# Kernel optimization log

Measured on AMD Instinct MI355X. Metric: run time of the kernel, lower is better.

The kernel has to match this reference:

```python
import jax, jax.numpy as jnp
import numpy as np

N_ROWS = 5000  # hard-coded loop bound in the source
N_FEAT = 20    # hard-coded x size in the source


def setup_inputs() -> dict:
    key = jax.random.key(0)
    kA, kb, kx = jax.random.split(key, 3)
    A = jax.random.normal(kA, (N_ROWS, N_FEAT), dtype=jnp.float32)
    b = jax.random.normal(kb, (N_ROWS,), dtype=jnp.float32)
    # nn.Parameter initialized as uniform(low=1, high=13, size=20)
    x = 1.0 + 12.0 * jax.random.uniform(kx, (N_FEAT,), dtype=jnp.float32)
    return {"A": A, "b": b, "x": x}


def reference(A, b, x):
    # Original: loss = sum_i ||A[i,:] @ x - b||^2, where the scalar A[i]@x
    # broadcasts against the full vector b each iteration.
    # Vectorized: s = A @ x (shape [N_ROWS]); residual r[i,j] = s[i] - b[j].
    s = A @ x                                   # [5000]
    r = s[:, None] - b[None, :]                  # [5000, 5000] broadcasted residual
    return jnp.sum(r * r)
```

## Files before the change

### kernel.cpp

```cpp
#include <hip/hip_runtime.h>
#include <hip/hip_bf16.h>


#define N_ROWS 5000
#define N_FEAT 20
#define NBLK   20
#define BLKSZ  256
#define NWAVES (BLKSZ / 64)

__device__ __forceinline__ double wave_reduce_sum(double v) {
    #pragma unroll
    for (int off = 32; off > 0; off >>= 1)
        v += __shfl_down(v, off, 64);
    return v;
}

__global__ __launch_bounds__(BLKSZ) void lsq_partial_kernel(
        const float* __restrict__ A, const float* __restrict__ b,
        const float* __restrict__ x, double* __restrict__ ws) {
    __shared__ float xs[N_FEAT];
    if (threadIdx.x < N_FEAT) xs[threadIdx.x] = x[threadIdx.x];
    __syncthreads();

    double s1 = 0.0, s2 = 0.0, b1 = 0.0, b2 = 0.0;
    int i = blockIdx.x * BLKSZ + threadIdx.x;
    if (i < N_ROWS) {
        const float4* __restrict__ row = (const float4*)(A + (long)i * N_FEAT);
        float4 r0 = row[0], r1 = row[1], r2 = row[2], r3 = row[3], r4 = row[4];
        float bv = b[i];
        float s = r0.x * xs[0]  + r0.y * xs[1]  + r0.z * xs[2]  + r0.w * xs[3]
                + r1.x * xs[4]  + r1.y * xs[5]  + r1.z * xs[6]  + r1.w * xs[7]
                + r2.x * xs[8]  + r2.y * xs[9]  + r2.z * xs[10] + r2.w * xs[11]
                + r3.x * xs[12] + r3.y * xs[13] + r3.z * xs[14] + r3.w * xs[15]
                + r4.x * xs[16] + r4.y * xs[17] + r4.z * xs[18] + r4.w * xs[19];
        s1 = (double)s;
        s2 = (double)s * (double)s;
        b1 = (double)bv;
        b2 = (double)bv * (double)bv;
    }

    s1 = wave_reduce_sum(s1);
    s2 = wave_reduce_sum(s2);
    b1 = wave_reduce_sum(b1);
    b2 = wave_reduce_sum(b2);

    __shared__ double red[NWAVES][4];
    int lane = threadIdx.x & 63;
    int wave = threadIdx.x >> 6;
    if (lane == 0) {
        red[wave][0] = s1; red[wave][1] = s2;
        red[wave][2] = b1; red[wave][3] = b2;
    }
    __syncthreads();
    if (threadIdx.x == 0) {
        double t0 = 0, t1 = 0, t2 = 0, t3 = 0;
        #pragma unroll
        for (int w = 0; w < NWAVES; ++w) {
            t0 += red[w][0]; t1 += red[w][1];
            t2 += red[w][2]; t3 += red[w][3];
        }
        double* p = ws + 4 * blockIdx.x;
        p[0] = t0; p[1] = t1; p[2] = t2; p[3] = t3;
    }
}

__global__ __launch_bounds__(64) void lsq_finalize_kernel(
        const double* __restrict__ ws, float* __restrict__ out) {
    double s1 = 0, s2 = 0, b1 = 0, b2 = 0;
    if (threadIdx.x < NBLK) {
        const double* p = ws + 4 * threadIdx.x;
        s1 = p[0]; s2 = p[1]; b1 = p[2]; b2 = p[3];
    }
    s1 = wave_reduce_sum(s1);
    s2 = wave_reduce_sum(s2);
    b1 = wave_reduce_sum(b1);
    b2 = wave_reduce_sum(b2);
    if (threadIdx.x == 0) {
        double n = (double)N_ROWS;
        out[0] = (float)(n * s2 - 2.0 * s1 * b1 + n * b2);
    }
}

extern "C" void kernel_launch(void* const* d_in, const int* in_sizes, int n_in,
                              void* d_out, int out_size, void* d_ws, size_t ws_size,
                              hipStream_t stream) {
    const float* A = (const float*)d_in[0];
    const float* b = (const float*)d_in[1];
    const float* x = (const float*)d_in[2];
    float* out = (float*)d_out;
    double* ws = (double*)d_ws;

    lsq_partial_kernel<<<NBLK, BLKSZ, 0, stream>>>(A, b, x, ws);
    lsq_finalize_kernel<<<1, 64, 0, stream>>>(ws, out);
}
```

Before: 58.88 us.

## Fuse partial and finalize kernels using complement-checksum handshake in workspace

After: 71.18 us. 1.21x slower.

```diff
diff --git a/kernel.cpp b/kernel.cpp
--- a/kernel.cpp
+++ b/kernel.cpp
@@ -1,5 +1,4 @@
 #include <hip/hip_runtime.h>
-#include <hip/hip_bf16.h>
 
 
 #define N_ROWS 5000
@@ -8,6 +7,8 @@
 #define BLKSZ  256
 #define NWAVES (BLKSZ / 64)
 
+typedef unsigned long long u64;
+
 __device__ __forceinline__ double wave_reduce_sum(double v) {
     #pragma unroll
     for (int off = 32; off > 0; off >>= 1)
@@ -15,69 +16,99 @@
     return v;
 }
 
-__global__ __launch_bounds__(BLKSZ) void lsq_partial_kernel(
+__device__ __forceinline__ u64 d2u(double d) { return __double_as_longlong(d); }
+__device__ __forceinline__ double u2d(u64 u) { return __longlong_as_double(u); }
+
+__global__ __launch_bounds__(BLKSZ) void lsq_fused_kernel(
         const float* __restrict__ A, const float* __restrict__ b,
-        const float* __restrict__ x, double* __restrict__ ws) {
-    __shared__ float xs[N_FEAT];
-    if (threadIdx.x < N_FEAT) xs[threadIdx.x] = x[threadIdx.x];
-    __syncthreads();
+        const float* __restrict__ x, u64* __restrict__ ws,
+        float* __restrict__ out) {
+    if (blockIdx.x < NBLK) {
+        double s1 = 0.0, s2 = 0.0, b1 = 0.0, b2 = 0.0;
+        int i = blockIdx.x * BLKSZ + threadIdx.x;
+        if (i < N_ROWS) {
+            const float4* __restrict__ row = (const float4*)(A + (long)i * N_FEAT);
+            float4 r0 = row[0], r1 = row[1], r2 = row[2], r3 = row[3], r4 = row[4];
+            float bv = b[i];
+            float s = r0.x * x[0]  + r0.y * x[1]  + r0.z * x[2]  + r0.w * x[3]
+                    + r1.x * x[4]  + r1.y * x[5]  + r1.z * x[6]  + r1.w * x[7]
+                    + r2.x * x[8]  + r2.y * x[9]  + r2.z * x[10] + r2.w * x[11]
+                    + r3.x * x[12] + r3.y * x[13] + r3.z * x[14] + r3.w * x[15]
+                    + r4.x * x[16] + r4.y * x[17] + r4.z * x[18] + r4.w * x[19];
+            s1 = (double)s;
+            s2 = (double)s * (double)s;
+            b1 = (double)bv;
+            b2 = (double)bv * (double)bv;
+        }
 
-    double s1 = 0.0, s2 = 0.0, b1 = 0.0, b2 = 0.0;
-    int i = blockIdx.x * BLKSZ + threadIdx.x;
-    if (i < N_ROWS) {
-        const float4* __restrict__ row = (const float4*)(A + (long)i * N_FEAT);
-        float4 r0 = row[0], r1 = row[1], r2 = row[2], r3 = row[3], r4 = row[4];
-        float bv = b[i];
-        float s = r0.x * xs[0]  + r0.y * xs[1]  + r0.z * xs[2]  + r0.w * xs[3]
-                + r1.x * xs[4]  + r1.y * xs[5]  + r1.z * xs[6]  + r1.w * xs[7]
-                + r2.x * xs[8]  + r2.y * xs[9]  + r2.z * xs[10] + r2.w * xs[11]
-                + r3.x * xs[12] + r3.y * xs[13] + r3.z * xs[14] + r3.w * xs[15]
-                + r4.x * xs[16] + r4.y * xs[17] + r4.z * xs[18] + r4.w * xs[19];
-        s1 = (double)s;
-        s2 = (double)s * (double)s;
-        b1 = (double)bv;
-        b2 = (double)bv * (double)bv;
-    }
+        s1 = wave_reduce_sum(s1);
+        s2 = wave_reduce_sum(s2);
+        b1 = wave_reduce_sum(b1);
+        b2 = wave_reduce_sum(b2);
 
-    s1 = wave_reduce_sum(s1);
-    s2 = wave_reduce_sum(s2);
-    b1 = wave_reduce_sum(b1);
-    b2 = wave_reduce_sum(b2);
+        __shared__ double red[NWAVES][4];
+        int lane = threadIdx.x & 63;
+        int wave = threadIdx.x >> 6;
+        if (lane == 0) {
+            red[wave][0] = s1; red[wave][1] = s2;
+            red[wave][2] = b1; red[wave][3] = b2;
+        }
+        __syncthreads();
+        if (threadIdx.x == 0) {
+            double t0 = 0, t1 = 0, t2 = 0, t3 = 0;
+            #pragma unroll
+            for (int w = 0; w < NWAVES; ++w) {
+                t0 += red[w][0]; t1 += red[w][1];
+                t2 += red[w][2]; t3 += red[w][3];
+            }
+            u64* p = ws + 8 * (u64)blockIdx.x;
+            u64 v0 = d2u(t0), v1 = d2u(t1), v2 = d2u(t2), v3 = d2u(t3);
+            __hip_atomic_store(&p[0], v0, __ATOMIC_RELAXED, __HIP_MEMORY_SCOPE_AGENT);
+            __hip_atomic_store(&p[1], v1, __ATOMIC_RELAXED, __HIP_MEMORY_SCOPE_AGENT);
+            __hip_atomic_store(&p[2], v2, __ATOMIC_RELAXED, __HIP_MEMORY_SCOPE_AGENT);
+            __hip_atomic_store(&p[3], v3, __ATOMIC_RELAXED, __HIP_MEMORY_SCOPE_AGENT);
+            __threadfence();
+            __hip_atomic_store(&p[4], ~v0, __ATOMIC_RELAXED, __HIP_MEMORY_SCOPE_AGENT);
+            __hip_atomic_store(&p[5], ~v1, __ATOMIC_RELAXED, __HIP_MEMORY_SCOPE_AGENT);
+            __hip_atomic_store(&p[6], ~v2, __ATOMIC_RELAXED, __HIP_MEMORY_SCOPE_AGENT);
+            __hip_atomic_store(&p[7], ~v3, __ATOMIC_RELAXED, __HIP_MEMORY_SCOPE_AGENT);
+        }
+    } else {
+        if (threadIdx.x == 0) {
+            bool done;
+            do {
+                done = true;
+                for (int blk = 0; blk < NBLK && done; ++blk) {
+                    const u64* p = ws + 8 * (u64)blk;
+                    #pragma unroll
+                    for (int k = 0; k < 4; ++k) {
+                        u64 v = __hip_atomic_load(&p[k],     __ATOMIC_RELAXED, __HIP_MEMORY_SCOPE_AGENT);
+                        u64 c = __hip_atomic_load(&p[4 + k], __ATOMIC_RELAXED, __HIP_MEMORY_SCOPE_AGENT);
+                        if (c != ~v) { done = false; break; }
+                    }
+                }
+                if (!done) __builtin_amdgcn_s_sleep(1);
+            } while (!done);
+            __threadfence();
+        }
+        __syncthreads();
 
-    __shared__ double red[NWAVES][4];
-    int lane = threadIdx.x & 63;
-    int wave = threadIdx.x >> 6;
-    if (lane == 0) {
-        red[wave][0] = s1; red[wave][1] = s2;
-        red[wave][2] = b1; red[wave][3] = b2;
-    }
-    __syncthreads();
-    if (threadIdx.x == 0) {
-        double t0 = 0, t1 = 0, t2 = 0, t3 = 0;
-        #pragma unroll
-        for (int w = 0; w < NWAVES; ++w) {
-            t0 += red[w][0]; t1 += red[w][1];
-            t2 += red[w][2]; t3 += red[w][3];
+        double s1 = 0, s2 = 0, b1 = 0, b2 = 0;
+        if (threadIdx.x < NBLK) {
+            const u64* p = ws + 8 * (u64)threadIdx.x;
+            s1 = u2d(__hip_atomic_load(&p[0], __ATOMIC_RELAXED, __HIP_MEMORY_SCOPE_AGENT));
+            s2 = u2d(__hip_atomic_load(&p[1], __ATOMIC_RELAXED, __HIP_MEMORY_SCOPE_AGENT));
+            b1 = u2d(__hip_atomic_load(&p[2], __ATOMIC_RELAXED, __HIP_MEMORY_SCOPE_AGENT));
+            b2 = u2d(__hip_atomic_load(&p[3], __ATOMIC_RELAXED, __HIP_MEMORY_SCOPE_AGENT));
         }
-        double* p = ws + 4 * blockIdx.x;
-        p[0] = t0; p[1] = t1; p[2] = t2; p[3] = t3;
-    }
-}
-
-__global__ __launch_bounds__(64) void lsq_finalize_kernel(
-        const double* __restrict__ ws, float* __restrict__ out) {
-    double s1 = 0, s2 = 0, b1 = 0, b2 = 0;
-    if (threadIdx.x < NBLK) {
-        const double* p = ws + 4 * threadIdx.x;
-        s1 = p[0]; s2 = p[1]; b1 = p[2]; b2 = p[3];
-    }
-    s1 = wave_reduce_sum(s1);
-    s2 = wave_reduce_sum(s2);
-    b1 = wave_reduce_sum(b1);
-    b2 = wave_reduce_sum(b2);
-    if (threadIdx.x == 0) {
-        double n = (double)N_ROWS;
-        out[0] = (float)(n * s2 - 2.0 * s1 * b1 + n * b2);
+        s1 = wave_reduce_sum(s1);
+        s2 = wave_reduce_sum(s2);
+        b1 = wave_reduce_sum(b1);
+        b2 = wave_reduce_sum(b2);
+        if (threadIdx.x == 0) {
+            double n = (double)N_ROWS;
+            out[0] = (float)(n * s2 - 2.0 * s1 * b1 + n * b2);
+        }
     }
 }
 
@@ -88,8 +119,7 @@
     const float* b = (const float*)d_in[1];
     const float* x = (const float*)d_in[2];
     float* out = (float*)d_out;
-    double* ws = (double*)d_ws;
+    u64* ws = (u64*)d_ws;
 
-    lsq_partial_kernel<<<NBLK, BLKSZ, 0, stream>>>(A, b, x, ws);
-    lsq_finalize_kernel<<<1, 64, 0, stream>>>(ws, out);
+    lsq_fused_kernel<<<NBLK + 1, BLKSZ, 0, stream>>>(A, b, x, ws, out);
 }
```
